# Performance work log

Measured on AMD Instinct MI355X. Metric: run time of the kernel, lower is better.

The kernel has to match this reference:

```python
import jax, jax.numpy as jnp
import numpy as np

S = 8192      # sequence length
D = 768       # bert_out_dim
NA = 256      # num aspects
NO = 256      # num opinions
MAXW = 40     # max span width (width_embedding has 40 entries)
NCAT = 13
NPOL = 3


def setup_inputs() -> dict:
    key = jax.random.key(0)
    ks = jax.random.split(key, 9)
    word_rep = jax.random.normal(ks[0], (S, D), jnp.float32)
    a_head = jax.random.randint(ks[1], (NA,), 0, S - MAXW)
    a_w = jax.random.randint(ks[2], (NA,), 1, MAXW + 1)
    aspects = jnp.stack([a_head, a_head + a_w], axis=-1)  # [NA,2] (head,tail), head<tail
    o_head = jax.random.randint(ks[3], (NO,), 0, S - MAXW)
    o_w = jax.random.randint(ks[4], (NO,), 1, MAXW + 1)
    opinions = jnp.stack([o_head, o_head + o_w], axis=-1)  # [NO,2]
    sc = 0.02
    return {
        'word_rep': word_rep,
        'aspects': aspects,
        'opinions': opinions,
        'W_valid': jax.random.normal(ks[5], (2 * D, 2), jnp.float32) * sc,
        'b_valid': jnp.zeros((2,), jnp.float32),
        'W_cat': jax.random.normal(ks[6], (2 * D, NCAT), jnp.float32) * sc,
        'b_cat': jnp.zeros((NCAT,), jnp.float32),
        'W_pol': jax.random.normal(ks[7], (2 * D, NPOL), jnp.float32) * sc,
        'b_pol': jnp.zeros((NPOL,), jnp.float32),
    }


def _span_maxpool(word_rep, spans):
    # variable-width span max-pool over tokens, vectorized with a gather + mask
    heads, tails = spans[:, 0], spans[:, 1]          # [n]
    pos = heads[:, None] + jnp.arange(MAXW)[None, :]  # [n, MAXW]
    valid = pos < tails[:, None]                      # [n, MAXW]
    g = word_rep[jnp.clip(pos, 0, word_rep.shape[0] - 1)]  # [n, MAXW, D]
    neg = jnp.finfo(word_rep.dtype).min
    return jnp.max(jnp.where(valid[:, :, None], g, neg), axis=1)  # [n, D]


def reference(word_rep, aspects, opinions, W_valid, b_valid, W_cat, b_cat, W_pol, b_pol):
    asp_rep = _span_maxpool(word_rep, aspects)   # [NA, D]
    opi_rep = _span_maxpool(word_rep, opinions)  # [NO, D]
    na, no = asp_rep.shape[0], opi_rep.shape[0]
    # all aspect x opinion pairs (itertools.product order): asp varies slowest
    pair_reps = jnp.concatenate([
        jnp.repeat(asp_rep, no, axis=0),          # [NA*NO, D]
        jnp.tile(opi_rep, (na, 1)),               # [NA*NO, D]
    ], axis=-1)                                    # [NA*NO, 2D]
    asp_ids = jnp.repeat(jnp.arange(na), no)
    opi_ids = jnp.tile(jnp.arange(no), na)

    valid_out = pair_reps @ W_valid + b_valid      # [P, 2]
    cate_out = pair_reps @ W_cat + b_cat           # [P, NCAT]
    polar_out = pair_reps @ W_pol + b_pol          # [P, NPOL]

    valid_mask = valid_out[:, 0] > valid_out[:, 1]  # [P] bool
    # jit-safe masking instead of data-dependent boolean select
    m = valid_mask[:, None]
    return (jnp.where(m, pair_reps, 0.0),
            jnp.where(valid_mask, asp_ids, -1),
            jnp.where(valid_mask, opi_ids, -1),
            jnp.where(m, cate_out, 0.0),
            jnp.where(m, polar_out, 0.0),
            valid_mask)
```

## Files before the change

kernel.cpp:

```cpp
#include <hip/hip_runtime.h>
#include <math.h>

#define S 8192
#define D 768
#define NA 256
#define NO 256
#define MAXW 40
#define NCAT 13
#define NPOL 3
#define NPROJ (2 + NCAT + NPOL)

#define OFF1 ((size_t)NA * NO * 2 * D)
#define OFF2 (OFF1 + (size_t)NA * NO)
#define OFF3 (OFF2 + (size_t)NA * NO)
#define OFF4 (OFF3 + (size_t)NA * NO * NCAT)
#define OFF5 (OFF4 + (size_t)NA * NO * NPOL)

#define NEGF (-3.402823466e+38f)

typedef float vfloat4 __attribute__((ext_vector_type(4)));

__global__ __launch_bounds__(256) void span_pool_proj(
    const float* __restrict__ word_rep,
    const int*   __restrict__ aspects,
    const int*   __restrict__ opinions,
    const float* __restrict__ W_valid,
    const float* __restrict__ W_cat,
    const float* __restrict__ W_pol,
    float*  __restrict__ rep_out,
    double* __restrict__ proj_out)
{
    __shared__ float  rep[D];
    __shared__ double part[4][NPROJ];
    const int b = blockIdx.x;
    const int t = threadIdx.x;

    const int* spans = (b < NA) ? aspects : opinions;
    const int  s     = (b < NA) ? b : (b - NA);
    const int  woff  = (b < NA) ? 0 : D;

    const int head  = spans[2 * s];
    const int tail  = spans[2 * s + 1];
    const int width = tail - head;

    if (t < 192) {
        const vfloat4* base = (const vfloat4*)(word_rep + (size_t)head * D) + t;
        vfloat4 m = base[0];
#pragma unroll
        for (int g = 0; g < MAXW; g += 8) {
            if (g && g >= width) break;
            const int rbeg = g ? g : 1;
#pragma unroll
            for (int r = rbeg; r < g + 8; ++r) {
                vfloat4 v = base[(size_t)r * (D / 4)];
                const bool ok = r < width;
                m.x = fmaxf(m.x, ok ? v.x : NEGF);
                m.y = fmaxf(m.y, ok ? v.y : NEGF);
                m.z = fmaxf(m.z, ok ? v.z : NEGF);
                m.w = fmaxf(m.w, ok ? v.w : NEGF);
            }
        }
        ((vfloat4*)rep)[t] = m;
        ((vfloat4*)(rep_out + (size_t)b * D))[t] = m;
    }
    __syncthreads();

    const int w    = t >> 6;
    const int lane = t & 63;
    if (lane < NPROJ) {
        const float* W; int ncol, col;
        if (lane < 2)           { W = W_valid; ncol = 2;    col = lane; }
        else if (lane < 2+NCAT) { W = W_cat;   ncol = NCAT; col = lane - 2; }
        else                    { W = W_pol;   ncol = NPOL; col = lane - 2 - NCAT; }
        const int d0 = w * (D / 4);
        double a0 = 0.0, a1 = 0.0;
#pragma unroll 8
        for (int d = d0; d < d0 + (D / 4); d += 2) {
            a0 += (double)rep[d]     * (double)W[(size_t)(woff + d)     * ncol + col];
            a1 += (double)rep[d + 1] * (double)W[(size_t)(woff + d + 1) * ncol + col];
        }
        part[w][lane] = a0 + a1;
    }
    __syncthreads();
    if (t < NPROJ)
        proj_out[(size_t)b * NPROJ + t] =
            (part[0][t] + part[1][t]) + (part[2][t] + part[3][t]);
}

#define JPB 64

__global__ __launch_bounds__(384) void pair_out(
    const vfloat4* __restrict__ rep4,
    const double*  __restrict__ proj,
    const float*   __restrict__ b_valid,
    const float*   __restrict__ b_cat,
    const float*   __restrict__ b_pol,
    float*         __restrict__ out)
{
    const int blk = blockIdx.x;
    const int i   = blk >> 2;
    const int j0  = (blk & 3) * JPB;
    const int t   = threadIdx.x;
    const int l   = t & 63;

    const double pa0 = proj[(size_t)i * NPROJ + 0];
    const double pa1 = proj[(size_t)i * NPROJ + 1];
    const double bv0 = (double)b_valid[0];
    const double bv1 = (double)b_valid[1];

    const double q0 = proj[(size_t)(NA + j0 + l) * NPROJ + 0];
    const double q1 = proj[(size_t)(NA + j0 + l) * NPROJ + 1];
    const unsigned long long mb = __ballot((pa0 + q0 + bv0) > (pa1 + q1 + bv1));

    vfloat4* dst = (vfloat4*)out + (size_t)((i << 8) | j0) * 384 + t;

    if (t < 192) {
        const vfloat4 av = rep4[(size_t)i * 192 + t];
#pragma unroll 8
        for (int jj = 0; jj < JPB; ++jj) {
            vfloat4 val = ((mb >> jj) & 1ULL) ? av : (vfloat4)0.f;
            dst[0] = val;
            dst += 384;
        }
    } else {
        const vfloat4* osrc = rep4 + (size_t)(NA + j0) * 192 + (t - 192);
#pragma unroll 8
        for (int jj = 0; jj < JPB; ++jj) {
            vfloat4 v   = osrc[0];
            vfloat4 val = ((mb >> jj) & 1ULL) ? v : (vfloat4)0.f;
            dst[0] = val;
            osrc += 192;
            dst  += 384;
        }
    }

    const int p0 = (i << 8) | j0;

    if (t < 208) {
        const int e0 = t * 4;
        vfloat4 v;
#pragma unroll
        for (int k = 0; k < 4; ++k) {
            const int e  = e0 + k;
            const int jj = e / NCAT;
            const int c  = e % NCAT;
            const bool mk = (mb >> jj) & 1ULL;
            const double pac = proj[(size_t)i * NPROJ + 2 + c];
            const double poc = proj[(size_t)(NA + j0 + jj) * NPROJ + 2 + c];
            v[k] = mk ? (float)(pac + poc + (double)b_cat[c]) : 0.0f;
        }
        *(vfloat4*)(out + OFF3 + (size_t)p0 * NCAT + e0) = v;
    } else if (t < 256) {
        const int e0 = (t - 208) * 4;
        vfloat4 v;
#pragma unroll
        for (int k = 0; k < 4; ++k) {
            const int e  = e0 + k;
            const int jj = e / NPOL;
            const int c  = e % NPOL;
            const bool mk = (mb >> jj) & 1ULL;
            const double pac = proj[(size_t)i * NPROJ + 2 + NCAT + c];
            const double poc = proj[(size_t)(NA + j0 + jj) * NPROJ + 2 + NCAT + c];
            v[k] = mk ? (float)(pac + poc + (double)b_pol[c]) : 0.0f;
        }
        *(vfloat4*)(out + OFF4 + (size_t)p0 * NPOL + e0) = v;
    } else if (t < 272) {
        const int e0 = (t - 256) * 4;
        vfloat4 v;
#pragma unroll
        for (int k = 0; k < 4; ++k)
            v[k] = ((mb >> (e0 + k)) & 1ULL) ? (float)i : -1.0f;
        *(vfloat4*)(out + OFF1 + (size_t)p0 + e0) = v;
    } else if (t < 288) {
        const int e0 = (t - 272) * 4;
        vfloat4 v;
#pragma unroll
        for (int k = 0; k < 4; ++k)
            v[k] = ((mb >> (e0 + k)) & 1ULL) ? (float)(j0 + e0 + k) : -1.0f;
        *(vfloat4*)(out + OFF2 + (size_t)p0 + e0) = v;
    } else if (t < 304) {
        const int e0 = (t - 288) * 4;
        vfloat4 v;
#pragma unroll
        for (int k = 0; k < 4; ++k)
            v[k] = ((mb >> (e0 + k)) & 1ULL) ? 1.0f : 0.0f;
        *(vfloat4*)(out + OFF5 + (size_t)p0 + e0) = v;
    }
}

extern "C" void kernel_launch(void* const* d_in, const int* in_sizes, int n_in,
                              void* d_out, int out_size, void* d_ws, size_t ws_size,
                              hipStream_t stream)
{
    const float* word_rep = (const float*)d_in[0];
    const int*   aspects  = (const int*)  d_in[1];
    const int*   opinions = (const int*)  d_in[2];
    const float* W_valid  = (const float*)d_in[3];
    const float* b_valid  = (const float*)d_in[4];
    const float* W_cat    = (const float*)d_in[5];
    const float* b_cat    = (const float*)d_in[6];
    const float* W_pol    = (const float*)d_in[7];
    const float* b_pol    = (const float*)d_in[8];
    float* out = (float*)d_out;

    float*  rep  = (float*)d_ws;
    double* proj = (double*)((char*)d_ws + (size_t)(NA + NO) * D * sizeof(float));

    span_pool_proj<<<NA + NO, 256, 0, stream>>>(
        word_rep, aspects, opinions, W_valid, W_cat, W_pol, rep, proj);

    pair_out<<<NA * 4, 384, 0, stream>>>(
        (const vfloat4*)rep, proj, b_valid, b_cat, b_pol, out);
}
```

Before: 446.1 us.

## Split span max-pool across two thread groups and use nontemporal pair stores

```diff
diff --git a/kernel.cpp b/kernel.cpp
--- a/kernel.cpp
+++ b/kernel.cpp
@@ -20,7 +20,7 @@
 
 typedef float vfloat4 __attribute__((ext_vector_type(4)));
 
-__global__ __launch_bounds__(256) void span_pool_proj(
+__global__ __launch_bounds__(384) void span_pool_proj(
     const float* __restrict__ word_rep,
     const int*   __restrict__ aspects,
     const int*   __restrict__ opinions,
@@ -30,8 +30,9 @@
     float*  __restrict__ rep_out,
     double* __restrict__ proj_out)
 {
-    __shared__ float  rep[D];
-    __shared__ double part[4][NPROJ];
+    __shared__ float   rep[D];
+    __shared__ vfloat4 part0[192];
+    __shared__ double  partp[6][NPROJ];
     const int b = blockIdx.x;
     const int t = threadIdx.x;
 
@@ -43,25 +44,36 @@
     const int tail  = spans[2 * s + 1];
     const int width = tail - head;
 
-    if (t < 192) {
-        const vfloat4* base = (const vfloat4*)(word_rep + (size_t)head * D) + t;
-        vfloat4 m = base[0];
-#pragma unroll
-        for (int g = 0; g < MAXW; g += 8) {
-            if (g && g >= width) break;
-            const int rbeg = g ? g : 1;
-#pragma unroll
-            for (int r = rbeg; r < g + 8; ++r) {
-                vfloat4 v = base[(size_t)r * (D / 4)];
-                const bool ok = r < width;
-                m.x = fmaxf(m.x, ok ? v.x : NEGF);
-                m.y = fmaxf(m.y, ok ? v.y : NEGF);
-                m.z = fmaxf(m.z, ok ? v.z : NEGF);
-                m.w = fmaxf(m.w, ok ? v.w : NEGF);
+    const int g = (t >= 192) ? 1 : 0;
+    const int c = g ? (t - 192) : t;
+
+    {
+        const vfloat4* base = (const vfloat4*)(word_rep + (size_t)head * D) + c;
+        vfloat4 m = (vfloat4)NEGF;
+#pragma unroll
+        for (int k = 0; k < MAXW / 2; ++k) {
+            if (k == 5 || k == 10 || k == 15) {
+                if (2 * k + g >= width) break;
             }
-        }
-        ((vfloat4*)rep)[t] = m;
-        ((vfloat4*)(rep_out + (size_t)b * D))[t] = m;
+            const int r = 2 * k + g;
+            vfloat4 v = base[(size_t)r * (D / 4)];
+            const bool ok = r < width;
+            m.x = fmaxf(m.x, ok ? v.x : NEGF);
+            m.y = fmaxf(m.y, ok ? v.y : NEGF);
+            m.z = fmaxf(m.z, ok ? v.z : NEGF);
+            m.w = fmaxf(m.w, ok ? v.w : NEGF);
+        }
+        if (!g) part0[c] = m;
+        __syncthreads();
+        if (g) {
+            vfloat4 p = part0[c];
+            m.x = fmaxf(m.x, p.x);
+            m.y = fmaxf(m.y, p.y);
+            m.z = fmaxf(m.z, p.z);
+            m.w = fmaxf(m.w, p.w);
+            ((vfloat4*)rep)[c] = m;
+            ((vfloat4*)(rep_out + (size_t)b * D))[c] = m;
+        }
     }
     __syncthreads();
 
@@ -72,19 +84,20 @@
         if (lane < 2)           { W = W_valid; ncol = 2;    col = lane; }
         else if (lane < 2+NCAT) { W = W_cat;   ncol = NCAT; col = lane - 2; }
         else                    { W = W_pol;   ncol = NPOL; col = lane - 2 - NCAT; }
-        const int d0 = w * (D / 4);
+        const int d0 = w * (D / 6);
         double a0 = 0.0, a1 = 0.0;
 #pragma unroll 8
-        for (int d = d0; d < d0 + (D / 4); d += 2) {
+        for (int d = d0; d < d0 + (D / 6); d += 2) {
             a0 += (double)rep[d]     * (double)W[(size_t)(woff + d)     * ncol + col];
             a1 += (double)rep[d + 1] * (double)W[(size_t)(woff + d + 1) * ncol + col];
         }
-        part[w][lane] = a0 + a1;
+        partp[w][lane] = a0 + a1;
     }
     __syncthreads();
     if (t < NPROJ)
         proj_out[(size_t)b * NPROJ + t] =
-            (part[0][t] + part[1][t]) + (part[2][t] + part[3][t]);
+            ((partp[0][t] + partp[1][t]) + (partp[2][t] + partp[3][t]))
+          +  (partp[4][t] + partp[5][t]);
 }
 
 #define JPB 64
@@ -119,7 +132,7 @@
 #pragma unroll 8
         for (int jj = 0; jj < JPB; ++jj) {
             vfloat4 val = ((mb >> jj) & 1ULL) ? av : (vfloat4)0.f;
-            dst[0] = val;
+            __builtin_nontemporal_store(val, dst);
             dst += 384;
         }
     } else {
@@ -128,7 +141,7 @@
         for (int jj = 0; jj < JPB; ++jj) {
             vfloat4 v   = osrc[0];
             vfloat4 val = ((mb >> jj) & 1ULL) ? v : (vfloat4)0.f;
-            dst[0] = val;
+            __builtin_nontemporal_store(val, dst);
             osrc += 192;
             dst  += 384;
         }
@@ -206,7 +219,7 @@
     float*  rep  = (float*)d_ws;
     double* proj = (double*)((char*)d_ws + (size_t)(NA + NO) * D * sizeof(float));
 
-    span_pool_proj<<<NA + NO, 256, 0, stream>>>(
+    span_pool_proj<<<NA + NO, 384, 0, stream>>>(
         word_rep, aspects, opinions, W_valid, W_cat, W_pol, rep, proj);
 
     pair_out<<<NA * 4, 384, 0, stream>>>(
```

Result: no change. 441.6 us (-1.0%).
